# Kernel tuning notes

Measured on AMD Instinct MI355X. Metric: run time of the kernel, lower is better.

## Reference

```python
import jax, jax.numpy as jnp
import numpy as np

D_MODEL = 1024
N_HEADS = 16
HEAD_DIM = D_MODEL // N_HEADS


def setup_inputs() -> dict:
    key = jax.random.key(0)
    ks = jax.random.split(key, 5)
    s = 1.0 / np.sqrt(D_MODEL)
    return {
        "x": jax.random.normal(ks[0], (2, 2048, D_MODEL), dtype=jnp.float32),
        "w_qkv": jax.random.uniform(ks[1], (3 * D_MODEL, D_MODEL), jnp.float32, -s, s),
        "b_qkv": jax.random.uniform(ks[2], (3 * D_MODEL,), jnp.float32, -s, s),
        "w_out": jax.random.uniform(ks[3], (D_MODEL, D_MODEL), jnp.float32, -s, s),
        "b_out": jax.random.uniform(ks[4], (D_MODEL,), jnp.float32, -s, s),
    }


def _attn(x, w_qkv, b_qkv, w_out, b_out):
    bsz, seq_len, _ = x.shape
    qkv = jnp.einsum('bsd,ed->bse', x, w_qkv) + b_qkv  # [B,S,3D]
    q, k, v = jnp.split(qkv, 3, axis=-1)
    def heads(t):  # [B,S,D] -> [B,H,S,Dh]
        return t.reshape(bsz, seq_len, N_HEADS, HEAD_DIM).transpose(0, 2, 1, 3)
    q, k, v = heads(q), heads(k), heads(v)
    scores = jnp.einsum('bhqd,bhkd->bhqk', q, k) / np.sqrt(HEAD_DIM)
    mask = jnp.tril(jnp.ones((seq_len, seq_len), dtype=bool))
    scores = jnp.where(mask, scores, -jnp.inf)
    probs = jax.nn.softmax(scores, axis=-1)
    attn = jnp.einsum('bhqk,bhkd->bhqd', probs, v)
    attn = attn.transpose(0, 2, 1, 3).reshape(bsz, seq_len, D_MODEL)
    return jnp.einsum('bsd,ed->bse', attn, w_out) + b_out


def reference(x, w_qkv, b_qkv, w_out, b_out):
    return _attn(x, w_qkv, b_qkv, w_out, b_out)
```

## Files before the change

kernel.cpp:

```cpp
#include <hip/hip_runtime.h>
#include <hip/hip_bf16.h>
#include <stdint.h>

#define SEQ     2048
#define BATCH   2
#define NHEADS  16
#define HDIM    64
#define DMODEL  1024
#define N3      3072
#define D2      2048
#define MTOT    (BATCH*SEQ)

typedef __attribute__((ext_vector_type(4))) float f32x4;
typedef __attribute__((ext_vector_type(8))) short bf16x8;

static __device__ inline unsigned short f2bf(float f) {
    union { float f; unsigned u; } v; v.f = f;
    unsigned r = (v.u + 0x7fffu + ((v.u >> 16) & 1u)) >> 16;
    return (unsigned short)r;
}
static __device__ inline unsigned pk2bf(float a, float b) {
    union { __hip_bfloat162 h; unsigned u; } c;
    c.h = __float22bfloat162_rn(make_float2(a, b));
    return c.u;
}

#define GLDS(gp, lp) __builtin_amdgcn_global_load_lds( \
    (const __attribute__((address_space(1))) void*)(gp), \
    (__attribute__((address_space(3))) void*)(lp), 16, 0, 0)

__global__ void cast_all(const float* __restrict__ x,
                         const float* __restrict__ wqkv,
                         const float* __restrict__ wout,
                         unsigned short* __restrict__ xb,
                         unsigned short* __restrict__ wqkvb,
                         unsigned short* __restrict__ woutb) {
    long i4 = (long)(blockIdx.x * blockDim.x + threadIdx.x) * 4;
    const float* src; unsigned short* dst; long off;
    if (i4 < 4194304L)      { src = x;    dst = xb;    off = i4; }
    else if (i4 < 7340032L) { src = wqkv; dst = wqkvb; off = i4 - 4194304L; }
    else                    { src = wout; dst = woutb; off = i4 - 7340032L; }
    float4 v = *(const float4*)(src + off);
    union { uint2 u; ushort4 s; } pk;
    pk.u.x = pk2bf(v.x, v.y); pk.u.y = pk2bf(v.z, v.w);
    *(ushort4*)(dst + off) = pk.s;
}

__global__ __launch_bounds__(512, 1) void gemm_qkv(
    const unsigned short* __restrict__ A,
    const unsigned short* __restrict__ B,
    const float* __restrict__ bias,
    unsigned short* __restrict__ qk,
    unsigned short* __restrict__ vT)
{
    __shared__ __align__(16) unsigned short sA[2][256][64];
    __shared__ __align__(16) unsigned short sB[2][256][64];
    const int tid  = threadIdx.x;
    const int w    = tid >> 6, lane = tid & 63;
    const int quad = lane >> 4, l16 = lane & 15, l7 = l16 & 7;
    const int wm = w >> 2, wn = w & 3;
    const int bid = blockIdx.x;
    const int m0 = (bid & 15) << 8;
    const int n0 = (bid >> 4) << 8;

    f32x4 acc[8][4];
    const f32x4 zero = {0.f, 0.f, 0.f, 0.f};
    #pragma unroll
    for (int i = 0; i < 8; i++)
        #pragma unroll
        for (int j = 0; j < 4; j++) acc[i][j] = zero;

    const int rsel = tid >> 3;
    const int sgl  = (tid & 7) ^ (rsel & 7);
    const unsigned short* gA = A + (long)(m0 + rsel) * 1024 + sgl * 8;
    const unsigned short* gB = B + (long)(n0 + rsel) * 1024 + sgl * 8;
    const int srow = w * 8;

    bf16x8 af[4][2];
    bf16x8 bfr[2][2][2];

    auto stageA = [&](int nb, int h, long ko) {
        GLDS(gA + (long)(h * 128)      * 1024 + ko, &sA[nb][h * 128 +      srow][0]);
        GLDS(gA + (long)(h * 128 + 64) * 1024 + ko, &sA[nb][h * 128 + 64 + srow][0]);
    };
    auto stageB = [&](int nb, int h, long ko) {
        GLDS(gB + (long)(h * 128)      * 1024 + ko, &sB[nb][h * 128 +      srow][0]);
        GLDS(gB + (long)(h * 128 + 64) * 1024 + ko, &sB[nb][h * 128 + 64 + srow][0]);
    };
    auto loadA = [&](int c, int mh) {
        #pragma unroll
        for (int mt2 = 0; mt2 < 4; mt2++)
            #pragma unroll
            for (int kk = 0; kk < 2; kk++)
                af[mt2][kk] = *(const bf16x8*)(
                    &sA[c][mh * 128 + wm * 64 + mt2 * 16 + l16]
                          [(((kk << 2) + quad) ^ l7) * 8]);
    };
    auto loadB = [&](int c, int nh) {
        #pragma unroll
        for (int nt2 = 0; nt2 < 2; nt2++)
            #pragma unroll
            for (int kk = 0; kk < 2; kk++)
                bfr[nh][nt2][kk] = *(const bf16x8*)(
                    &sB[c][nh * 128 + wn * 32 + nt2 * 16 + l16]
                          [(((kk << 2) + quad) ^ l7) * 8]);
    };
    auto mfmaQ = [&](int mh, int nh) {
        __builtin_amdgcn_s_setprio(1);
        #pragma unroll
        for (int mt2 = 0; mt2 < 4; mt2++)
            #pragma unroll
            for (int nt2 = 0; nt2 < 2; nt2++)
                #pragma unroll
                for (int kk = 0; kk < 2; kk++)
                    acc[mh * 4 + mt2][nh * 2 + nt2] =
                        __builtin_amdgcn_mfma_f32_16x16x32_bf16(
                            af[mt2][kk], bfr[nh][nt2][kk],
                            acc[mh * 4 + mt2][nh * 2 + nt2], 0, 0, 0);
        __builtin_amdgcn_s_setprio(0);
    };

    stageB(0, 0, 0); stageB(0, 1, 0); stageA(0, 0, 0); stageA(0, 1, 0);
    __builtin_amdgcn_sched_barrier(0);
    asm volatile("s_waitcnt vmcnt(2)" ::: "memory");
    __builtin_amdgcn_sched_barrier(0);
    __builtin_amdgcn_s_barrier();

    for (int t = 0; t < 15; ++t) {
        const int c = t & 1, nb = c ^ 1;
        const long ko = (long)(t + 1) * 64;

        loadA(c, 0); loadB(c, 0);
        stageB(nb, 0, ko);
        __builtin_amdgcn_s_barrier();
        asm volatile("s_waitcnt lgkmcnt(0)" ::: "memory");
        __builtin_amdgcn_sched_barrier(0);
        mfmaQ(0, 0);
        __builtin_amdgcn_sched_barrier(0);
        __builtin_amdgcn_s_barrier();

        loadB(c, 1);
        stageB(nb, 1, ko);
        __builtin_amdgcn_sched_barrier(0);
        asm volatile("s_waitcnt vmcnt(4)" ::: "memory");
        __builtin_amdgcn_sched_barrier(0);
        __builtin_amdgcn_s_barrier();
        asm volatile("s_waitcnt lgkmcnt(0)" ::: "memory");
        __builtin_amdgcn_sched_barrier(0);
        mfmaQ(0, 1);
        __builtin_amdgcn_sched_barrier(0);
        __builtin_amdgcn_s_barrier();

        loadA(c, 1);
        stageA(nb, 0, ko);
        __builtin_amdgcn_s_barrier();
        asm volatile("s_waitcnt lgkmcnt(0)" ::: "memory");
        __builtin_amdgcn_sched_barrier(0);
        mfmaQ(1, 1);
        __builtin_amdgcn_sched_barrier(0);
        __builtin_amdgcn_s_barrier();

        stageA(nb, 1, ko);
        __builtin_amdgcn_sched_barrier(0);
        asm volatile("s_waitcnt vmcnt(2)" ::: "memory");
        __builtin_amdgcn_sched_barrier(0);
        __builtin_amdgcn_s_barrier();
        mfmaQ(1, 0);
        __builtin_amdgcn_sched_barrier(0);
        __builtin_amdgcn_s_barrier();
    }
    {
        const int c = 1;
        loadA(c, 0); loadB(c, 0);
        __builtin_amdgcn_s_barrier();
        asm volatile("s_waitcnt lgkmcnt(0)" ::: "memory");
        __builtin_amdgcn_sched_barrier(0);
        mfmaQ(0, 0);
        __builtin_amdgcn_sched_barrier(0);
        __builtin_amdgcn_s_barrier();

        loadB(c, 1);
        __builtin_amdgcn_sched_barrier(0);
        asm volatile("s_waitcnt vmcnt(0)" ::: "memory");
        __builtin_amdgcn_sched_barrier(0);
        __builtin_amdgcn_s_barrier();
        asm volatile("s_waitcnt lgkmcnt(0)" ::: "memory");
        __builtin_amdgcn_sched_barrier(0);
        mfmaQ(0, 1);
        __builtin_amdgcn_sched_barrier(0);
        __builtin_amdgcn_s_barrier();

        loadA(c, 1);
        __builtin_amdgcn_s_barrier();
        asm volatile("s_waitcnt lgkmcnt(0)" ::: "memory");
        __builtin_amdgcn_sched_barrier(0);
        mfmaQ(1, 1);
        mfmaQ(1, 0);
    }

    if (n0 < 2048) {
        #pragma unroll
        for (int ni = 0; ni < 4; ni++) {
            const int n_g = n0 + (ni >> 1) * 128 + wn * 32 + (ni & 1) * 16 + l16;
            const float bv = bias[n_g];
            #pragma unroll
            for (int mi = 0; mi < 8; mi++) {
                const int mb = (mi >> 2) * 128 + wm * 64 + (mi & 3) * 16 + quad * 4;
                #pragma unroll
                for (int r = 0; r < 4; r++) {
                    const int m_g = m0 + mb + r;
                    qk[(long)m_g * D2 + n_g] = f2bf(acc[mi][ni][r] + bv);
                }
            }
        }
    } else {
        const int b = m0 >> 11;
        #pragma unroll
        for (int ni = 0; ni < 4; ni++) {
            const int n_g = n0 + (ni >> 1) * 128 + wn * 32 + (ni & 1) * 16 + l16;
            const int dm = n_g - 2048;
            const long vrow = (long)(((b << 4) + (dm >> 6)) << 6) + (dm & 63);
            const float bv = bias[n_g];
            #pragma unroll
            for (int mi = 0; mi < 8; mi++) {
                const int m_g = m0 + (mi >> 2) * 128 + wm * 64 + (mi & 3) * 16 + quad * 4;
                union { uint2 u; ushort4 s; } pk;
                pk.u.x = pk2bf(acc[mi][ni][0] + bv, acc[mi][ni][1] + bv);
                pk.u.y = pk2bf(acc[mi][ni][2] + bv, acc[mi][ni][3] + bv);
                *(ushort4*)(vT + vrow * D2 + (m_g & 2047)) = pk.s;
            }
        }
    }
}

__global__ __launch_bounds__(256, 2) void gemm_out(
    const unsigned short* __restrict__ A,
    const unsigned short* __restrict__ B,
    const float* __restrict__ bias,
    float* __restrict__ C)
{
    __shared__ __align__(16) unsigned short sA[2][128][64];
    __shared__ __align__(16) unsigned short sB[2][64][64];
    const int tid  = threadIdx.x;
    const int wave = tid >> 6, lane = tid & 63;
    const int quad = lane >> 4, l16 = lane & 15, l7 = l16 & 7;
    const int wm = wave >> 1, wn = wave & 1;
    const int m0 = blockIdx.x * 128, n0 = blockIdx.y * 64;

    f32x4 acc[4][2];
    const f32x4 zero = {0.f, 0.f, 0.f, 0.f};
    #pragma unroll
    for (int i = 0; i < 4; i++) { acc[i][0] = zero; acc[i][1] = zero; }

    const int rsel = tid >> 3;
    const int sgl  = (tid & 7) ^ (rsel & 7);
    const unsigned short* gA0 = A + (long)(m0 + rsel) * 1024 + sgl * 8;
    const unsigned short* gB0 = B + (long)(n0 + rsel) * 1024 + sgl * 8;

    #pragma unroll
    for (int i = 0; i < 4; i++)
        GLDS(gA0 + (long)(32 * i) * 1024, &sA[0][32 * i + wave * 8][0]);
    #pragma unroll
    for (int i = 0; i < 2; i++)
        GLDS(gB0 + (long)(32 * i) * 1024, &sB[0][32 * i + wave * 8][0]);

    int buf = 0;
    for (int k0 = 0; k0 < 1024; k0 += 64, buf ^= 1) {
        __syncthreads();
        if (k0 + 64 < 1024) {
            #pragma unroll
            for (int i = 0; i < 4; i++)
                GLDS(gA0 + (long)(32 * i) * 1024 + k0 + 64, &sA[buf ^ 1][32 * i + wave * 8][0]);
            #pragma unroll
            for (int i = 0; i < 2; i++)
                GLDS(gB0 + (long)(32 * i) * 1024 + k0 + 64, &sB[buf ^ 1][32 * i + wave * 8][0]);
        }
        #pragma unroll
        for (int ks = 0; ks < 2; ks++) {
            bf16x8 af[4], bfr[2];
            #pragma unroll
            for (int mt = 0; mt < 4; mt++)
                af[mt] = *(const bf16x8*)(&sA[buf][wm * 64 + mt * 16 + l16][((ks * 4 + quad) ^ l7) * 8]);
            #pragma unroll
            for (int nt = 0; nt < 2; nt++)
                bfr[nt] = *(const bf16x8*)(&sB[buf][wn * 32 + nt * 16 + l16][((ks * 4 + quad) ^ l7) * 8]);
            #pragma unroll
            for (int mt = 0; mt < 4; mt++)
                #pragma unroll
                for (int nt = 0; nt < 2; nt++)
                    acc[mt][nt] = __builtin_amdgcn_mfma_f32_16x16x32_bf16(
                        af[mt], bfr[nt], acc[mt][nt], 0, 0, 0);
        }
    }
    #pragma unroll
    for (int nt = 0; nt < 2; nt++) {
        const int n_g = n0 + wn * 32 + nt * 16 + l16;
        const float bv = bias[n_g];
        #pragma unroll
        for (int mt = 0; mt < 4; mt++) {
            #pragma unroll
            for (int r = 0; r < 4; r++) {
                const int m_g = m0 + wm * 64 + mt * 16 + quad * 4 + r;
                C[(long)m_g * DMODEL + n_g] = acc[mt][nt][r] + bv;
            }
        }
    }
}

__global__ __launch_bounds__(512, 1) void attn_kernel(
    const unsigned short* __restrict__ qk,
    const unsigned short* __restrict__ vT,
    unsigned short* __restrict__ attn)
{
    __shared__ __align__(16) unsigned short sK [2][2][64][64];
    __shared__ __align__(16) unsigned short sVt[2][2][64][64];
    __shared__ __align__(16) unsigned short sP [8][16][64];

    const int tid  = threadIdx.x;
    const int w    = tid >> 6, lane = tid & 63;
    const int quad = lane >> 4, l16 = lane & 15, l7 = l16 & 7;

    const int bh = blockIdx.x;
    const int b  = bh >> 4, h = bh & 15;
    const int pair = blockIdx.y;
    const long rowb = (long)b * SEQ;

    const int rl = lane >> 3;
    const int sm = (lane & 7) ^ rl;
    const unsigned short* kg = qk + (rowb + w * 8 + rl) * D2 + 1024 + h * HDIM + sm * 8;
    const unsigned short* vg = vT + (long)(bh * 64 + w * 8 + rl) * D2 + sm * 8;

    const int s0 = quad ^ l7;
    const float C2 = 0.18033688011112042f;
    const f32x4 zero = {0.f, 0.f, 0.f, 0.f};

    #pragma unroll
    for (int ph = 0; ph < 2; ph++) {
        const int qtile  = ph ? (15 - pair) : pair;
        const int qbase  = qtile * 128;
        const int ntiles = 2 * qtile + 2;
        const int npairs = ntiles >> 1;

        bf16x8 qf0, qf1;
        {
            const unsigned short* qp = qk + (rowb + qbase + w * 16 + l16) * D2 + h * HDIM;
            qf0 = *(const bf16x8*)(qp + quad * 8);
            qf1 = *(const bf16x8*)(qp + 32 + quad * 8);
        }
        f32x4 Oacc[4];
        #pragma unroll
        for (int mf = 0; mf < 4; mf++) Oacc[mf] = zero;
        float l_i = 0.f;

        __syncthreads();
        {
            GLDS(kg,            &sK [0][0][w * 8][0]);
            GLDS(vg,            &sVt[0][0][w * 8][0]);
            GLDS(kg + 64L * D2, &sK [0][1][w * 8][0]);
            GLDS(vg + 64,       &sVt[0][1][w * 8][0]);
        }

        int buf = 0;
        for (int p = 0; p < npairs; p++, buf ^= 1) {
            __syncthreads();
            if (p + 1 < npairs) {
                const long o0 = (long)(2 * p + 2) * 64;
                const long o1 = (long)(2 * p + 3) * 64;
                GLDS(kg + o0 * D2, &sK [buf ^ 1][0][w * 8][0]);
                GLDS(vg + o0,      &sVt[buf ^ 1][0][w * 8][0]);
                GLDS(kg + o1 * D2, &sK [buf ^ 1][1][w * 8][0]);
                GLDS(vg + o1,      &sVt[buf ^ 1][1][w * 8][0]);
            }
            #pragma unroll
            for (int s = 0; s < 2; s++) {
                const int t = 2 * p + s;

                f32x4 st[4];
                __builtin_amdgcn_s_setprio(1);
                #pragma unroll
                for (int kvf = 0; kvf < 4; kvf++) {
                    bf16x8 kf0 = *(const bf16x8*)(&sK[buf][s][kvf * 16 + l16][s0 * 8]);
                    bf16x8 kf1 = *(const bf16x8*)(&sK[buf][s][kvf * 16 + l16][(s0 ^ 4) * 8]);
                    st[kvf] = __builtin_amdgcn_mfma_f32_16x16x32_bf16(kf0, qf0, zero, 0, 0, 0);
                    st[kvf] = __builtin_amdgcn_mfma_f32_16x16x32_bf16(kf1, qf1, st[kvf], 0, 0, 0);
                }
                __builtin_amdgcn_s_setprio(0);
                if (t >= 2 * qtile) {
                    const int ql = w * 16 + l16;
                    const int tb = (t - 2 * qtile) * 64;
                    #pragma unroll
                    for (int kvf = 0; kvf < 4; kvf++) {
                        const int kv = tb + kvf * 16 + quad * 4;
                        #pragma unroll
                        for (int r = 0; r < 4; r++)
                            if (kv + r > ql) st[kvf][r] = -1e30f;
                    }
                }
                #pragma unroll
                for (int kvf = 0; kvf < 4; kvf++) {
                    #pragma unroll
                    for (int r = 0; r < 4; r++)
                        st[kvf][r] = __builtin_amdgcn_exp2f(st[kvf][r] * C2);
                }
                f32x4 ps = (st[0] + st[1]) + (st[2] + st[3]);
                l_i += (ps[0] + ps[1]) + (ps[2] + ps[3]);

                #pragma unroll
                for (int kvf = 0; kvf < 4; kvf++) {
                    union { uint2 u; ushort4 s4; } pk;
                    pk.u.x = pk2bf(st[kvf][0], st[kvf][1]);
                    pk.u.y = pk2bf(st[kvf][2], st[kvf][3]);
                    const int seg = (kvf * 2 + (quad >> 1)) ^ l7;
                    *(ushort4*)(&sP[w][l16][seg * 8 + (quad & 1) * 4]) = pk.s4;
                }
                bf16x8 pf0 = *(const bf16x8*)(&sP[w][l16][(quad ^ l7) * 8]);
                bf16x8 pf1 = *(const bf16x8*)(&sP[w][l16][((4 + quad) ^ l7) * 8]);
                __builtin_amdgcn_s_setprio(1);
                #pragma unroll
                for (int mf = 0; mf < 4; mf++) {
                    bf16x8 vf0 = *(const bf16x8*)(&sVt[buf][s][mf * 16 + l16][s0 * 8]);
                    bf16x8 vf1 = *(const bf16x8*)(&sVt[buf][s][mf * 16 + l16][(s0 ^ 4) * 8]);
                    Oacc[mf] = __builtin_amdgcn_mfma_f32_16x16x32_bf16(vf0, pf0, Oacc[mf], 0, 0, 0);
                    Oacc[mf] = __builtin_amdgcn_mfma_f32_16x16x32_bf16(vf1, pf1, Oacc[mf], 0, 0, 0);
                }
                __builtin_amdgcn_s_setprio(0);
            }
        }
        float L = l_i;
        L += __shfl_xor(L, 16);
        L += __shfl_xor(L, 32);
        const float inv = 1.0f / L;
        const int q = qbase + w * 16 + l16;
        unsigned short* op = attn + (rowb + q) * DMODEL + h * HDIM + quad * 4;
        #pragma unroll
        for (int mf = 0; mf < 4; mf++) {
            union { uint2 u; ushort4 s4; } pk;
            pk.u.x = pk2bf(Oacc[mf][0] * inv, Oacc[mf][1] * inv);
            pk.u.y = pk2bf(Oacc[mf][2] * inv, Oacc[mf][3] * inv);
            *(ushort4*)(op + mf * 16) = pk.s4;
        }
    }
}

extern "C" void kernel_launch(void* const* d_in, const int* in_sizes, int n_in,
                              void* d_out, int out_size, void* d_ws, size_t ws_size,
                              hipStream_t stream) {
    const float* x    = (const float*)d_in[0];
    const float* wqkv = (const float*)d_in[1];
    const float* bqkv = (const float*)d_in[2];
    const float* wout = (const float*)d_in[3];
    const float* bout = (const float*)d_in[4];

    char* ws = (char*)d_ws;
    unsigned short* xb    = (unsigned short*)(ws);
    unsigned short* wqkvb = (unsigned short*)(ws + (8L << 20));
    unsigned short* woutb = (unsigned short*)(ws + (14L << 20));
    unsigned short* qkb   = (unsigned short*)(ws + (16L << 20));
    unsigned short* vTb   = (unsigned short*)(ws + (32L << 20));
    unsigned short* attnb = (unsigned short*)(ws + (40L << 20));

    cast_all<<<8192, 256, 0, stream>>>(x, wqkv, wout, xb, wqkvb, woutb);

    gemm_qkv<<<192, 512, 0, stream>>>(xb, wqkvb, bqkv, qkb, vTb);

    dim3 g2(32, 8);
    attn_kernel<<<g2, 512, 0, stream>>>(qkb, vTb, attnb);

    dim3 g3(32, 16);
    gemm_out<<<g3, 256, 0, stream>>>(attnb, woutb, bout, (float*)d_out);
}
```

Measured before the change: 171.4 us.

## Shrink QKV GEMM N-tile to 192 so grid fills 256 CUs

Changes the QKV projection GEMM tile from 256x256 to 256x192, raising the grid from 192 to 256 workgroups so every CU on the device gets one block. The inner pipeline is restructured into three 64-column B slices with reordered MFMA groups, and one barrier/wait point is folded into MFMA work to overlap loads with compute. The epilogue now decides per column whether output goes to qk or transposed V, since a tile can straddle the boundary. Smaller tiles lower arithmetic intensity per block, and the rebuilt waitcnt sequence could be slightly off.

```diff
diff --git a/kernel.cpp b/kernel.cpp
--- a/kernel.cpp
+++ b/kernel.cpp
@@ -54,21 +54,21 @@
     unsigned short* __restrict__ vT)
 {
     __shared__ __align__(16) unsigned short sA[2][256][64];
-    __shared__ __align__(16) unsigned short sB[2][256][64];
+    __shared__ __align__(16) unsigned short sB[2][192][64];
     const int tid  = threadIdx.x;
     const int w    = tid >> 6, lane = tid & 63;
     const int quad = lane >> 4, l16 = lane & 15, l7 = l16 & 7;
     const int wm = w >> 2, wn = w & 3;
     const int bid = blockIdx.x;
     const int m0 = (bid & 15) << 8;
-    const int n0 = (bid >> 4) << 8;
-
-    f32x4 acc[8][4];
+    const int n0 = (bid >> 4) * 192;
+
+    f32x4 acc[8][3];
     const f32x4 zero = {0.f, 0.f, 0.f, 0.f};
     #pragma unroll
     for (int i = 0; i < 8; i++)
         #pragma unroll
-        for (int j = 0; j < 4; j++) acc[i][j] = zero;
+        for (int j = 0; j < 3; j++) acc[i][j] = zero;
 
     const int rsel = tid >> 3;
     const int sgl  = (tid & 7) ^ (rsel & 7);
@@ -77,50 +77,45 @@
     const int srow = w * 8;
 
     bf16x8 af[4][2];
-    bf16x8 bfr[2][2][2];
+    bf16x8 bfr[3][2];
 
     auto stageA = [&](int nb, int h, long ko) {
         GLDS(gA + (long)(h * 128)      * 1024 + ko, &sA[nb][h * 128 +      srow][0]);
         GLDS(gA + (long)(h * 128 + 64) * 1024 + ko, &sA[nb][h * 128 + 64 + srow][0]);
     };
-    auto stageB = [&](int nb, int h, long ko) {
-        GLDS(gB + (long)(h * 128)      * 1024 + ko, &sB[nb][h * 128 +      srow][0]);
-        GLDS(gB + (long)(h * 128 + 64) * 1024 + ko, &sB[nb][h * 128 + 64 + srow][0]);
+    auto stageB = [&](int nb, int j, long ko) {
+        GLDS(gB + (long)(j * 64) * 1024 + ko, &sB[nb][j * 64 + srow][0]);
     };
     auto loadA = [&](int c, int mh) {
         #pragma unroll
-        for (int mt2 = 0; mt2 < 4; mt2++)
+        for (int mt = 0; mt < 4; mt++)
             #pragma unroll
             for (int kk = 0; kk < 2; kk++)
-                af[mt2][kk] = *(const bf16x8*)(
-                    &sA[c][mh * 128 + wm * 64 + mt2 * 16 + l16]
+                af[mt][kk] = *(const bf16x8*)(
+                    &sA[c][mh * 128 + wm * 64 + mt * 16 + l16]
                           [(((kk << 2) + quad) ^ l7) * 8]);
     };
-    auto loadB = [&](int c, int nh) {
-        #pragma unroll
-        for (int nt2 = 0; nt2 < 2; nt2++)
+    auto loadB = [&](int c, int ns) {
+        #pragma unroll
+        for (int kk = 0; kk < 2; kk++)
+            bfr[ns][kk] = *(const bf16x8*)(
+                &sB[c][ns * 64 + wn * 16 + l16]
+                      [(((kk << 2) + quad) ^ l7) * 8]);
+    };
+    auto mfmaP = [&](int mh, int ns) {
+        __builtin_amdgcn_s_setprio(1);
+        #pragma unroll
+        for (int mt = 0; mt < 4; mt++)
             #pragma unroll
             for (int kk = 0; kk < 2; kk++)
-                bfr[nh][nt2][kk] = *(const bf16x8*)(
-                    &sB[c][nh * 128 + wn * 32 + nt2 * 16 + l16]
-                          [(((kk << 2) + quad) ^ l7) * 8]);
-    };
-    auto mfmaQ = [&](int mh, int nh) {
-        __builtin_amdgcn_s_setprio(1);
-        #pragma unroll
-        for (int mt2 = 0; mt2 < 4; mt2++)
-            #pragma unroll
-            for (int nt2 = 0; nt2 < 2; nt2++)
-                #pragma unroll
-                for (int kk = 0; kk < 2; kk++)
-                    acc[mh * 4 + mt2][nh * 2 + nt2] =
-                        __builtin_amdgcn_mfma_f32_16x16x32_bf16(
-                            af[mt2][kk], bfr[nh][nt2][kk],
-                            acc[mh * 4 + mt2][nh * 2 + nt2], 0, 0, 0);
+                acc[mh * 4 + mt][ns] =
+                    __builtin_amdgcn_mfma_f32_16x16x32_bf16(
+                        af[mt][kk], bfr[ns][kk], acc[mh * 4 + mt][ns], 0, 0, 0);
         __builtin_amdgcn_s_setprio(0);
     };
 
-    stageB(0, 0, 0); stageB(0, 1, 0); stageA(0, 0, 0); stageA(0, 1, 0);
+    stageB(0, 0, 0); stageB(0, 1, 0); stageB(0, 2, 0);
+    stageA(0, 0, 0); stageA(0, 1, 0);
     __builtin_amdgcn_sched_barrier(0);
     asm volatile("s_waitcnt vmcnt(2)" ::: "memory");
     __builtin_amdgcn_sched_barrier(0);
@@ -135,19 +130,18 @@
         __builtin_amdgcn_s_barrier();
         asm volatile("s_waitcnt lgkmcnt(0)" ::: "memory");
         __builtin_amdgcn_sched_barrier(0);
-        mfmaQ(0, 0);
-        __builtin_amdgcn_sched_barrier(0);
-        __builtin_amdgcn_s_barrier();
-
-        loadB(c, 1);
-        stageB(nb, 1, ko);
-        __builtin_amdgcn_sched_barrier(0);
-        asm volatile("s_waitcnt vmcnt(4)" ::: "memory");
-        __builtin_amdgcn_sched_barrier(0);
-        __builtin_amdgcn_s_barrier();
-        asm volatile("s_waitcnt lgkmcnt(0)" ::: "memory");
-        __builtin_amdgcn_sched_barrier(0);
-        mfmaQ(0, 1);
+        mfmaP(0, 0);
+        __builtin_amdgcn_sched_barrier(0);
+        __builtin_amdgcn_s_barrier();
+
+        loadB(c, 1); loadB(c, 2);
+        stageB(nb, 1, ko); stageB(nb, 2, ko);
+        __builtin_amdgcn_s_barrier();
+        asm volatile("s_waitcnt lgkmcnt(0)" ::: "memory");
+        __builtin_amdgcn_sched_barrier(0);
+        mfmaP(0, 1); mfmaP(0, 2);
+        __builtin_amdgcn_sched_barrier(0);
+        asm volatile("s_waitcnt vmcnt(3)" ::: "memory");
         __builtin_amdgcn_sched_barrier(0);
         __builtin_amdgcn_s_barrier();
 
@@ -156,16 +150,15 @@
         __builtin_amdgcn_s_barrier();
         asm volatile("s_waitcnt lgkmcnt(0)" ::: "memory");
         __builtin_amdgcn_sched_barrier(0);
-        mfmaQ(1, 1);
+        mfmaP(1, 2); mfmaP(1, 1);
         __builtin_amdgcn_sched_barrier(0);
         __builtin_amdgcn_s_barrier();
 
         stageA(nb, 1, ko);
         __builtin_amdgcn_sched_barrier(0);
+        mfmaP(1, 0);
+        __builtin_amdgcn_sched_barrier(0);
         asm volatile("s_waitcnt vmcnt(2)" ::: "memory");
-        __builtin_amdgcn_sched_barrier(0);
-        __builtin_amdgcn_s_barrier();
-        mfmaQ(1, 0);
         __builtin_amdgcn_sched_barrier(0);
         __builtin_amdgcn_s_barrier();
     }
@@ -175,34 +168,31 @@
         __builtin_amdgcn_s_barrier();
         asm volatile("s_waitcnt lgkmcnt(0)" ::: "memory");
         __builtin_amdgcn_sched_barrier(0);
-        mfmaQ(0, 0);
-        __builtin_amdgcn_sched_barrier(0);
-        __builtin_amdgcn_s_barrier();
-
-        loadB(c, 1);
+        mfmaP(0, 0);
+        __builtin_amdgcn_sched_barrier(0);
+        __builtin_amdgcn_s_barrier();
+
+        loadB(c, 1); loadB(c, 2);
+        __builtin_amdgcn_s_barrier();
+        asm volatile("s_waitcnt lgkmcnt(0)" ::: "memory");
+        __builtin_amdgcn_sched_barrier(0);
+        mfmaP(0, 1); mfmaP(0, 2);
         __builtin_amdgcn_sched_barrier(0);
         asm volatile("s_waitcnt vmcnt(0)" ::: "memory");
         __builtin_amdgcn_sched_barrier(0);
         __builtin_amdgcn_s_barrier();
-        asm volatile("s_waitcnt lgkmcnt(0)" ::: "memory");
-        __builtin_amdgcn_sched_barrier(0);
-        mfmaQ(0, 1);
-        __builtin_amdgcn_sched_barrier(0);
-        __builtin_amdgcn_s_barrier();
 
         loadA(c, 1);
-        __builtin_amdgcn_s_barrier();
-        asm volatile("s_waitcnt lgkmcnt(0)" ::: "memory");
-        __builtin_amdgcn_sched_barrier(0);
-        mfmaQ(1, 1);
-        mfmaQ(1, 0);
-    }
-
-    if (n0 < 2048) {
-        #pragma unroll
-        for (int ni = 0; ni < 4; ni++) {
-            const int n_g = n0 + (ni >> 1) * 128 + wn * 32 + (ni & 1) * 16 + l16;
-            const float bv = bias[n_g];
+        asm volatile("s_waitcnt lgkmcnt(0)" ::: "memory");
+        __builtin_amdgcn_sched_barrier(0);
+        mfmaP(1, 2); mfmaP(1, 1); mfmaP(1, 0);
+    }
+
+    #pragma unroll
+    for (int ni = 0; ni < 3; ni++) {
+        const int n_g = n0 + ni * 64 + wn * 16 + l16;
+        const float bv = bias[n_g];
+        if (n_g < 2048) {
             #pragma unroll
             for (int mi = 0; mi < 8; mi++) {
                 const int mb = (mi >> 2) * 128 + wm * 64 + (mi & 3) * 16 + quad * 4;
@@ -212,15 +202,10 @@
                     qk[(long)m_g * D2 + n_g] = f2bf(acc[mi][ni][r] + bv);
                 }
             }
-        }
-    } else {
-        const int b = m0 >> 11;
-        #pragma unroll
-        for (int ni = 0; ni < 4; ni++) {
-            const int n_g = n0 + (ni >> 1) * 128 + wn * 32 + (ni & 1) * 16 + l16;
+        } else {
+            const int b = m0 >> 11;
             const int dm = n_g - 2048;
-            const long vrow = (long)(((b << 4) + (dm >> 6)) << 6) + (dm & 63);
-            const float bv = bias[n_g];
+            const long vrow = (long)b * 1024 + dm;
             #pragma unroll
             for (int mi = 0; mi < 8; mi++) {
                 const int m_g = m0 + (mi >> 2) * 128 + wm * 64 + (mi & 3) * 16 + quad * 4;
@@ -461,7 +446,7 @@
 
     cast_all<<<8192, 256, 0, stream>>>(x, wqkv, wout, xb, wqkvb, woutb);
 
-    gemm_qkv<<<192, 512, 0, stream>>>(xb, wqkvb, bqkv, qkb, vTb);
+    gemm_qkv<<<256, 512, 0, stream>>>(xb, wqkvb, bqkv, qkb, vTb);
 
     dim3 g2(32, 8);
     attn_kernel<<<g2, 512, 0, stream>>>(qkb, vTb, attnb);
```

Result: faster. 167.9 us (-2.0%).
